# Optimization experiments

Hardware: AMD Instinct MI355X
Metric: run time of the kernel (lower is better)

## Reference

```python
import jax, jax.numpy as jnp
import numpy as np

B, N, D, H, FN, NL = 8, 512, 128, 64, 3, 3
OUT = 10


def setup_inputs() -> dict:
    key = jax.random.key(0)
    ks = jax.random.split(key, 20)
    X = jax.random.normal(ks[0], (B, N, D), dtype=jnp.float32)
    a = jax.random.uniform(ks[1], (B, N, N))
    A = (a < 0.02).astype(jnp.float32)
    A = jnp.maximum(A, jnp.swapaxes(A, 1, 2)) * (1.0 - jnp.eye(N, dtype=jnp.float32))
    w = lambda k, s: jax.random.normal(k, s, dtype=jnp.float32) * 0.05
    z = lambda s: jnp.zeros(s, jnp.float32)
    return {
        'X': X, 'A': A, 'p': 10,
        'curv_W1': w(ks[2], (D, H)), 'curv_b1': z((H,)),
        'curv_W2': w(ks[3], (H, 1)), 'curv_b2': z((1,)),
        'wm_W1': w(ks[4], (1, 64)), 'wm_b1': z((64,)),
        'wm_W2': w(ks[5], (64, 32)), 'wm_b2': z((32,)),
        'wm_W3': w(ks[6], (32, 1)), 'wm_b3': z((1,)),
        'fn_W1': w(ks[7], (FN, D, H)), 'fn_b1': z((FN, H)),
        'fn_W2': w(ks[8], (FN, H, 1)), 'fn_b2': z((FN, 1)),
        'gin_eps': z((NL,)),
        'gin0_W1': w(ks[9], (D, H)), 'gin0_b1': z((H,)),
        'gin0_W2': w(ks[10], (H, H)), 'gin0_b2': z((H,)),
        'gin1_W1': w(ks[11], (H, H)), 'gin1_b1': z((H,)),
        'gin1_W2': w(ks[12], (H, H)), 'gin1_b2': z((H,)),
        'gin2_W1': w(ks[13], (H, H)), 'gin2_b1': z((H,)),
        'gin2_W2': w(ks[14], (H, H)), 'gin2_b2': z((H,)),
        'out_W': w(ks[15], (D + H * NL, OUT)), 'out_b': z((OUT,)),
    }


def _curv_mlp(x, W1, b1, W2, b2):
    # MLP(nfeat->nhid->1) followed by sigmoid
    return jax.nn.sigmoid(jax.nn.relu(x @ W1 + b1) @ W2 + b2)


def _weight_mlp(A, W1, b1, W2, b2, W3, b3):
    # per-entry scalar MLP over adjacency: [B,N,N] -> [B,N,N]
    x = jax.nn.relu(A[..., None] * W1[0] + b1)  # [B,N,N,64]
    x = jax.nn.relu(x @ W2 + b2)                # [B,N,N,32]
    return jax.nn.sigmoid(x @ W3 + b3)[..., 0]


def _mv(w, v):
    return jnp.einsum('bij,bj->bi', w, v)


def _curvature_terms(f, w):
    # Algebraically identical to the torch O(N^2) expanded version, but
    # expressed with matvec contractions to avoid redundant [B,N,N] temps.
    deg = w.sum(axis=2)
    wf = _mv(w, f)
    # gamma_i = 0.5 sum_j w_ij (f_j - f_i)^2
    gamma = 0.5 * (f * f * deg - 2.0 * f * wf + _mv(w, f * f))
    # delta_f_i = sum_j w_ij (f_i - f_j)
    delta_f = f * deg - wf
    # delta_gamma_i = sum_j w_ij (gamma_i - gamma_j)
    delta_gamma = gamma * deg - _mv(w, gamma)
    # gfd_i = 0.5 sum_j w_ij (f_i - f_j)(delta_f_i - delta_f_j)
    gfd = 0.5 * (f * delta_f * deg - f * _mv(w, delta_f)
                 - delta_f * wf + _mv(w, f * delta_f))
    gamma2 = 0.5 * delta_gamma - gfd
    return gamma, gamma2


def _prune(A, kap, pct):
    num = int(N * pct / 100)  # static under jit (pct is a Python int)
    _, idx = jax.lax.top_k(kap, num)
    mask = jnp.ones((B, N), A.dtype).at[jnp.arange(B)[:, None], idx].set(0.0)
    return A * mask[:, :, None] * mask[:, None, :]


def _forward(X, A, curv_W1, curv_b1, curv_W2, curv_b2,
             wm_W1, wm_b1, wm_W2, wm_b2, wm_W3, wm_b3,
             fn_W1, fn_b1, fn_W2, fn_b2, gin_eps,
             gin0_W1, gin0_b1, gin0_W2, gin0_b2,
             gin1_W1, gin1_b1, gin1_W2, gin1_b2,
             gin2_W1, gin2_b1, gin2_W2, gin2_b2,
             out_W, out_b, p):
    kappa = _curv_mlp(X, curv_W1, curv_b1, curv_W2, curv_b2)  # [B,N,1]
    kap = kappa[..., 0]
    weights = _weight_mlp(A, wm_W1, wm_b1, wm_W2, wm_b2, wm_W3, wm_b3) * A
    curv_loss = jnp.float32(0.0)
    for i in range(FN):
        f = _curv_mlp(X, fn_W1[i], fn_b1[i], fn_W2[i], fn_b2[i])[..., 0]
        gamma, gamma2 = _curvature_terms(f, weights)
        curv_loss = curv_loss + jax.nn.relu(kap * gamma - gamma2).sum() - kappa.sum()
    gins = [(gin0_W1, gin0_b1, gin0_W2, gin0_b2),
            (gin1_W1, gin1_b1, gin1_W2, gin1_b2),
            (gin2_W1, gin2_b1, gin2_W2, gin2_b2)]
    h, A_cur, hiddens = X, A, [X]
    for t in range(NL):
        W1, b1, W2, b2 = gins[t]
        # GIN: MLP((1+eps) x + A x); dropout is identity (eval/deterministic)
        agg = (1.0 + gin_eps[t]) * h + jnp.einsum('bij,bjd->bid', A_cur, h)
        h = jax.nn.relu(jax.nn.relu(agg @ W1 + b1) @ W2 + b2)
        A_cur = _prune(A_cur, kap, p * (t + 1))
        hiddens.append(h)
    out = jnp.concatenate(hiddens, axis=2).sum(axis=1) @ out_W + out_b
    return out, curv_loss


def reference(X, A, p, curv_W1, curv_b1, curv_W2, curv_b2,
              wm_W1, wm_b1, wm_W2, wm_b2, wm_W3, wm_b3,
              fn_W1, fn_b1, fn_W2, fn_b2, gin_eps,
              gin0_W1, gin0_b1, gin0_W2, gin0_b2,
              gin1_W1, gin1_b1, gin1_W2, gin1_b2,
              gin2_W1, gin2_b1, gin2_W2, gin2_b2,
              out_W, out_b):
    return _forward(X, A, curv_W1, curv_b1, curv_W2, curv_b2,
                    wm_W1, wm_b1, wm_W2, wm_b2, wm_W3, wm_b3,
                    fn_W1, fn_b1, fn_W2, fn_b2, gin_eps,
                    gin0_W1, gin0_b1, gin0_W2, gin0_b2,
                    gin1_W1, gin1_b1, gin1_W2, gin1_b2,
                    gin2_W1, gin2_b1, gin2_W2, gin2_b2,
                    out_W, out_b, p)
```

## Files before the change

kernel.cpp:

```cpp
#include <hip/hip_runtime.h>
#include <math.h>

#define BATCH 8
#define NNODE 512
#define BN 4096
#define DIM 128
#define HID 64
#define CAP 64

__device__ __forceinline__ float sigmoidf(float x) {
  return 1.f / (1.f + expf(-x));
}
__device__ __forceinline__ float wave_sum(float v) {
  for (int off = 1; off < 64; off <<= 1) v += __shfl_xor(v, off, 64);
  return v;
}

template <int CIN, bool MASKED, int SOFF>
__device__ __forceinline__ void gin_block(
    float* smem, int node0, const float* hin, const float* W1g,
    const float* b1, const float* W2g, const float* b2, float eps1,
    const int* csr, const int* cnt, const float* mask, float* hout,
    float* Ssum) {
  float* W1s = smem;
  float* aggs = smem + CIN * HID;
  float* zs = aggs + 8 * CIN;
  int tid = threadIdx.x, wave = tid >> 6, lane = tid & 63;
  for (int t = tid; t < CIN * HID / 4; t += 256)
    ((float4*)W1s)[t] = ((const float4*)W1g)[t];
  for (int i = 0; i < 2; i++) {
    int ln = wave * 2 + i;
    int r = node0 + ln;
    int b9 = r & ~(NNODE - 1);
    const float* hi = hin + (size_t)r * CIN;
    float a0 = eps1 * hi[lane];
    float a1 = (CIN == 128) ? eps1 * hi[lane + 64] : 0.f;
    int n = cnt[r];
    const int* nb = csr + r * CAP;
    float mrow = MASKED ? mask[r] : 1.f;
    float s0 = 0.f, s1 = 0.f;
    for (int t = 0; t < n; t += 8) {
      int4 ja = *(const int4*)&nb[t];
      int4 jb = *(const int4*)&nb[t + 4];
      int r0 = b9 + ja.x, r1 = b9 + ja.y, r2 = b9 + ja.z, r3 = b9 + ja.w;
      int r4 = b9 + jb.x, r5 = b9 + jb.y, r6 = b9 + jb.z, r7 = b9 + jb.w;
      float m0 = MASKED ? mask[r0] : 1.f;
      float m1 = (t + 1 < n) ? (MASKED ? mask[r1] : 1.f) : 0.f;
      float m2 = (t + 2 < n) ? (MASKED ? mask[r2] : 1.f) : 0.f;
      float m3 = (t + 3 < n) ? (MASKED ? mask[r3] : 1.f) : 0.f;
      float m4 = (t + 4 < n) ? (MASKED ? mask[r4] : 1.f) : 0.f;
      float m5 = (t + 5 < n) ? (MASKED ? mask[r5] : 1.f) : 0.f;
      float m6 = (t + 6 < n) ? (MASKED ? mask[r6] : 1.f) : 0.f;
      float m7 = (t + 7 < n) ? (MASKED ? mask[r7] : 1.f) : 0.f;
      const float* p0 = hin + (size_t)r0 * CIN;
      const float* p1 = hin + (size_t)r1 * CIN;
      const float* p2 = hin + (size_t)r2 * CIN;
      const float* p3 = hin + (size_t)r3 * CIN;
      const float* p4 = hin + (size_t)r4 * CIN;
      const float* p5 = hin + (size_t)r5 * CIN;
      const float* p6 = hin + (size_t)r6 * CIN;
      const float* p7 = hin + (size_t)r7 * CIN;
      s0 += m0 * p0[lane] + m1 * p1[lane] + m2 * p2[lane] + m3 * p3[lane] +
            m4 * p4[lane] + m5 * p5[lane] + m6 * p6[lane] + m7 * p7[lane];
      if (CIN == 128)
        s1 += m0 * p0[lane + 64] + m1 * p1[lane + 64] + m2 * p2[lane + 64] +
              m3 * p3[lane + 64] + m4 * p4[lane + 64] + m5 * p5[lane + 64] +
              m6 * p6[lane + 64] + m7 * p7[lane + 64];
    }
    a0 += mrow * s0;
    if (CIN == 128) a1 += mrow * s1;
    aggs[ln * CIN + lane] = a0;
    if (CIN == 128) aggs[ln * CIN + 64 + lane] = a1;
  }
  __syncthreads();
  const float* x0 = aggs + (wave * 2 + 0) * CIN;
  const float* x1 = aggs + (wave * 2 + 1) * CIN;
  float bb = b1[lane];
  float acc0 = bb, acc1 = bb;
  for (int k = 0; k < CIN; k += 4) {
    float w0 = W1s[(k + 0) * HID + lane];
    float w1 = W1s[(k + 1) * HID + lane];
    float w2 = W1s[(k + 2) * HID + lane];
    float w3 = W1s[(k + 3) * HID + lane];
    float4 a;
    a = *(const float4*)&x0[k];
    acc0 += a.x * w0 + a.y * w1 + a.z * w2 + a.w * w3;
    a = *(const float4*)&x1[k];
    acc1 += a.x * w0 + a.y * w1 + a.z * w2 + a.w * w3;
  }
  zs[(wave * 2 + 0) * HID + lane] = fmaxf(0.f, acc0);
  zs[(wave * 2 + 1) * HID + lane] = fmaxf(0.f, acc1);
  const float* z0 = zs + (wave * 2 + 0) * HID;
  const float* z1 = zs + (wave * 2 + 1) * HID;
  float b2b = b2[lane];
  float c0 = b2b, c1v = b2b;
  for (int k = 0; k < HID; k += 4) {
    float w0 = W2g[(k + 0) * HID + lane];
    float w1 = W2g[(k + 1) * HID + lane];
    float w2 = W2g[(k + 2) * HID + lane];
    float w3 = W2g[(k + 3) * HID + lane];
    float4 a;
    a = *(const float4*)&z0[k];
    c0 += a.x * w0 + a.y * w1 + a.z * w2 + a.w * w3;
    a = *(const float4*)&z1[k];
    c1v += a.x * w0 + a.y * w1 + a.z * w2 + a.w * w3;
  }
  float h0 = fmaxf(0.f, c0), h1v = fmaxf(0.f, c1v);
  size_t rb = (size_t)(node0 + wave * 2) * HID + lane;
  hout[rb + 0 * HID] = h0;
  hout[rb + 1 * HID] = h1v;
  zs[(wave * 2) * HID + lane] = h0 + h1v;
  __syncthreads();
  if (tid < HID) {
    float tot = zs[0 * HID + tid] + zs[2 * HID + tid] + zs[4 * HID + tid] +
                zs[6 * HID + tid];
    atomicAdd(&Ssum[(node0 >> 9) * 320 + SOFF + tid], tot);
  }
}

__global__ __launch_bounds__(256) void k_stage1(
    const float* X, const float* A, const float* cW1, const float* cb1,
    const float* cW2, const float* cb2, const float* fW1, const float* fb1,
    const float* fW2, const float* fb2, const float* wm_W1, const float* wm_b1,
    const float* wm_W2, const float* wm_b2, const float* wm_W3,
    const float* wm_b3, float* kap, float* f, float* c1_out, int* csr,
    int* cnt_arr, float* deg, float* Ssum) {
  __shared__ float smem[10240];
  int bid = blockIdx.x;
  int tid = threadIdx.x, wave = tid >> 6, lane = tid & 63;
  if (bid < 1024) {
    int m = bid >> 8;
    int grp = bid & 255;
    float* W1s = smem;
    float* xs = smem + 8192;
    int node0 = grp * 16;
    const float* W1 = (m == 0) ? cW1 : fW1 + (size_t)(m - 1) * DIM * HID;
    for (int t = tid; t < 16 * DIM / 4; t += 256)
      ((float4*)xs)[t] = ((const float4*)(X + (size_t)node0 * DIM))[t];
    for (int t = tid; t < DIM * HID / 4; t += 256)
      ((float4*)W1s)[t] = ((const float4*)W1)[t];
    __syncthreads();
    const float* b1 = (m == 0) ? cb1 : fb1 + (m - 1) * HID;
    const float* W2 = (m == 0) ? cW2 : fW2 + (m - 1) * HID;
    float b2v = (m == 0) ? cb2[0] : fb2[m - 1];
    const float* x0 = xs + (wave * 4 + 0) * DIM;
    const float* x1 = xs + (wave * 4 + 1) * DIM;
    const float* x2 = xs + (wave * 4 + 2) * DIM;
    const float* x3 = xs + (wave * 4 + 3) * DIM;
    float w2l = W2[lane];
    float bb = b1[lane];
    float acc0 = bb, acc1 = bb, acc2 = bb, acc3 = bb;
    for (int k = 0; k < DIM; k += 4) {
      float w0 = W1s[(k + 0) * HID + lane];
      float w1 = W1s[(k + 1) * HID + lane];
      float w2 = W1s[(k + 2) * HID + lane];
      float w3 = W1s[(k + 3) * HID + lane];
      float4 a;
      a = *(const float4*)&x0[k];
      acc0 += a.x * w0 + a.y * w1 + a.z * w2 + a.w * w3;
      a = *(const float4*)&x1[k];
      acc1 += a.x * w0 + a.y * w1 + a.z * w2 + a.w * w3;
      a = *(const float4*)&x2[k];
      acc2 += a.x * w0 + a.y * w1 + a.z * w2 + a.w * w3;
      a = *(const float4*)&x3[k];
      acc3 += a.x * w0 + a.y * w1 + a.z * w2 + a.w * w3;
    }
    float s0 = wave_sum(fmaxf(0.f, acc0) * w2l);
    float s1 = wave_sum(fmaxf(0.f, acc1) * w2l);
    float s2 = wave_sum(fmaxf(0.f, acc2) * w2l);
    float s3 = wave_sum(fmaxf(0.f, acc3) * w2l);
    if (lane < 4) {
      float sv = (lane == 0) ? s0 : (lane == 1) ? s1 : (lane == 2) ? s2 : s3;
      float s = sigmoidf(sv + b2v);
      int node = node0 + wave * 4 + lane;
      if (m == 0) kap[node] = s;
      else f[node * 3 + (m - 1)] = s;
    }
    return;
  }
  if (bid < 2048) {
    int r = (bid - 1024) * 4 + wave;
    const float* row = A + (size_t)r * NNODE;
    int base = r * CAP, cnt = 0;
    for (int c = 0; c < NNODE / 64; c++) {
      int j = c * 64 + lane;
      bool nz = (row[j] != 0.f);
      unsigned long long mb = __ballot(nz);
      if (nz) {
        int pos = __popcll(mb & ((1ull << lane) - 1ull));
        int slot = cnt + pos;
        if (slot < CAP) csr[base + slot] = j;
      }
      cnt += (int)__popcll(mb);
    }
    int cc = cnt < CAP ? cnt : CAP;
    if (lane >= cc) csr[base + lane] = 0;
    if (lane == 0) {
      cnt_arr[r] = cc;
      deg[r] = (float)cnt;
    }
    return;
  }
  for (int t = tid; t < BATCH * 320; t += 256) Ssum[t] = 0.f;
  float* u = smem;
  float* y = smem + 64;
  int l = tid;
  if (l < 64) u[l] = fmaxf(0.f, wm_W1[l] + wm_b1[l]);
  __syncthreads();
  if (l < 32) {
    float a = wm_b2[l];
    for (int k = 0; k < 64; k++) a += u[k] * wm_W2[k * 32 + l];
    y[l] = fmaxf(0.f, a);
  }
  __syncthreads();
  if (l == 0) {
    float a = wm_b3[0];
    for (int k = 0; k < 32; k++) a += y[k] * wm_W3[k];
    *c1_out = sigmoidf(a);
  }
}

__global__ __launch_bounds__(256) void k_stage2(
    const float* X, const float* f, const float* kap, const int* p_ptr,
    const int* csr, const int* cnt, const float* deg, const float* c1p,
    const float* g0_W1, const float* g0_b1, const float* g0_W2,
    const float* g0_b2, const float* gin_eps, float* GG, float* M1, float* M2,
    float* h1, float* Ssum) {
  __shared__ float smem[9728];
  int bid = blockIdx.x;
  int wave = threadIdx.x >> 6, lane = threadIdx.x & 63;
  if (bid < 1024) {
    int r = bid * 4 + wave;
    int b9 = r & ~(NNODE - 1);
    int n = cnt[r];
    int j = csr[r * CAP + lane];
    float f0 = 0.f, f1 = 0.f, f2 = 0.f;
    if (lane < n) {
      const float* fj = f + (size_t)(b9 + j) * 3;
      f0 = fj[0]; f1 = fj[1]; f2 = fj[2];
    }
    float s10 = wave_sum(f0), s11 = wave_sum(f1), s12 = wave_sum(f2);
    float s20 = wave_sum(f0 * f0), s21 = wave_sum(f1 * f1),
          s22 = wave_sum(f2 * f2);
    if (lane < 3) {
      float s1 = (lane == 0) ? s10 : (lane == 1) ? s11 : s12;
      float s2 = (lane == 0) ? s20 : (lane == 1) ? s21 : s22;
      float c1 = *c1p, dA = deg[r];
      float fi = f[r * 3 + lane];
      float gamma = 0.5f * c1 * (fi * fi * dA - 2.f * fi * s1 + s2);
      float df = c1 * (fi * dA - s1);
      float* o = GG + (size_t)r * 12;
      o[lane * 3 + 0] = gamma;
      o[lane * 3 + 1] = df;
      o[lane * 3 + 2] = fi * df;
      o[9 + lane] = s1;
    }
    return;
  }
  if (bid < 1024 + BATCH) {
    int b = bid - 1024;
    float* ks = smem;
    for (int t = threadIdx.x; t < NNODE; t += 256) ks[t] = kap[b * NNODE + t];
    __syncthreads();
    int p = *p_ptr;
    int num1 = (NNODE * p) / 100;
    int num2 = (NNODE * 2 * p) / 100;
    int numm = num1 > num2 ? num1 : num2;
    for (int i = threadIdx.x; i < NNODE; i += 256) {
      float v = ks[i];
      int rank = 0;
      for (int j = 0; j < NNODE; j++) {
        float u = ks[j];
        rank += (u > v) || (u == v && j < i);
      }
      M1[b * NNODE + i] = (rank < num1) ? 0.f : 1.f;
      M2[b * NNODE + i] = (rank < numm) ? 0.f : 1.f;
    }
    return;
  }
  if (bid < 1024 + BATCH + 512) {
    gin_block<DIM, false, 128>(smem, (bid - 1024 - BATCH) * 8, X, g0_W1,
                               g0_b1, g0_W2, g0_b2, 1.f + gin_eps[0], csr,
                               cnt, nullptr, h1, Ssum);
    return;
  }
  int idx = bid - (1024 + BATCH + 512);
  int b = idx >> 3, sl = idx & 7;
  int col = threadIdx.x & 127, rg = threadIdx.x >> 7;
  const float* xb = X + (size_t)b * NNODE * DIM;
  int n0 = sl * 64;
  float s = 0.f;
  for (int n = n0 + rg; n < n0 + 64; n += 2) s += xb[(size_t)n * DIM + col];
  smem[threadIdx.x] = s;
  __syncthreads();
  if (threadIdx.x < 128)
    atomicAdd(&Ssum[b * 320 + col], smem[threadIdx.x] + smem[threadIdx.x + 128]);
}

__global__ __launch_bounds__(256) void k_stage3(
    const float* f, const float* kap, const float* deg, const float* GG,
    const int* csr, const int* cnt, const float* c1p, float* loss_part,
    const float* h1, const float* g1_W1, const float* g1_b1,
    const float* g1_W2, const float* g1_b2, const float* gin_eps,
    const float* M1, float* h2, float* Ssum) {
  __shared__ float smem[5120];
  __shared__ float part[4];
  int bid = blockIdx.x;
  int wave = threadIdx.x >> 6, lane = threadIdx.x & 63;
  if (bid < 1024) {
    int r = bid * 4 + wave;
    int b9 = r & ~(NNODE - 1);
    int n = cnt[r];
    int j = csr[r * CAP + lane];
    float T[9];
    for (int c = 0; c < 9; c++) T[c] = 0.f;
    if (lane < n) {
      const float4* g = (const float4*)(GG + (size_t)(b9 + j) * 12);
      float4 g0 = g[0], g1 = g[1], g2 = g[2];
      T[0] = g0.x; T[1] = g0.y; T[2] = g0.z;
      T[3] = g0.w; T[4] = g1.x; T[5] = g1.y;
      T[6] = g1.z; T[7] = g1.w; T[8] = g2.x;
    }
    for (int c = 0; c < 9; c++) T[c] = wave_sum(T[c]);
    float kp = kap[r];
    float local = 0.f;
    if (lane < 3) {
      int i = lane;
      float c1 = *c1p, dA = deg[r];
      const float* o = GG + (size_t)r * 12;
      float fi = f[r * 3 + i];
      float s1 = o[9 + i];
      float gamma = o[i * 3 + 0], df = o[i * 3 + 1];
      float dgamma = c1 * (gamma * dA - T[i * 3 + 0]);
      float gfd = 0.5f * c1 * (fi * df * dA - fi * T[i * 3 + 1] - df * s1 +
                               T[i * 3 + 2]);
      float gamma2 = 0.5f * dgamma - gfd;
      local = fmaxf(0.f, kp * gamma - gamma2);
    }
    if (lane == 0) local -= 3.f * kp;
    local = wave_sum(local);
    if (lane == 0) part[wave] = local;
    __syncthreads();
    if (threadIdx.x == 0)
      loss_part[bid] = part[0] + part[1] + part[2] + part[3];
    return;
  }
  gin_block<HID, true, 192>(smem, (bid - 1024) * 8, h1, g1_W1, g1_b1, g1_W2,
                            g1_b2, 1.f + gin_eps[1], csr, cnt, M1, h2, Ssum);
}

__global__ __launch_bounds__(256) void k_stage4(
    const float* h2, const float* g2_W1, const float* g2_b1,
    const float* g2_W2, const float* g2_b2, const float* gin_eps,
    const int* csr, const int* cnt, const float* M2, float* h3, float* Ssum) {
  __shared__ float smem[5120];
  gin_block<HID, true, 256>(smem, blockIdx.x * 8, h2, g2_W1, g2_b1, g2_W2,
                            g2_b2, 1.f + gin_eps[2], csr, cnt, M2, h3, Ssum);
}

__global__ __launch_bounds__(320) void k_out(
    const float* Ssum, const float* out_W, const float* out_b,
    const float* loss_part, float* out) {
  int b = blockIdx.x;
  int t = threadIdx.x;
  __shared__ float S[320];
  __shared__ float wpart[5];
  S[t] = Ssum[b * 320 + t];
  if (b == 0) {
    float ls = 0.f;
    for (int i = t; i < 1024; i += 320) ls += loss_part[i];
    ls = wave_sum(ls);
    if ((t & 63) == 0) wpart[t >> 6] = ls;
  }
  __syncthreads();
  if (t < 10) {
    float acc = out_b[t];
    for (int d = 0; d < 320; d++) acc += S[d] * out_W[d * 10 + t];
    out[b * 10 + t] = acc;
  }
  if (b == 0 && t == 0) {
    float ls = 0.f;
    for (int w = 0; w < 5; w++) ls += wpart[w];
    out[80] = ls;
  }
}

extern "C" void kernel_launch(void* const* d_in, const int* in_sizes, int n_in,
                              void* d_out, int out_size, void* d_ws,
                              size_t ws_size, hipStream_t stream) {
  const float* X       = (const float*)d_in[0];
  const float* A       = (const float*)d_in[1];
  const int*   p       = (const int*)d_in[2];
  const float* curv_W1 = (const float*)d_in[3];
  const float* curv_b1 = (const float*)d_in[4];
  const float* curv_W2 = (const float*)d_in[5];
  const float* curv_b2 = (const float*)d_in[6];
  const float* wm_W1   = (const float*)d_in[7];
  const float* wm_b1   = (const float*)d_in[8];
  const float* wm_W2   = (const float*)d_in[9];
  const float* wm_b2   = (const float*)d_in[10];
  const float* wm_W3   = (const float*)d_in[11];
  const float* wm_b3   = (const float*)d_in[12];
  const float* fn_W1   = (const float*)d_in[13];
  const float* fn_b1   = (const float*)d_in[14];
  const float* fn_W2   = (const float*)d_in[15];
  const float* fn_b2   = (const float*)d_in[16];
  const float* gin_eps = (const float*)d_in[17];
  const float* g0_W1   = (const float*)d_in[18];
  const float* g0_b1   = (const float*)d_in[19];
  const float* g0_W2   = (const float*)d_in[20];
  const float* g0_b2   = (const float*)d_in[21];
  const float* g1_W1   = (const float*)d_in[22];
  const float* g1_b1   = (const float*)d_in[23];
  const float* g1_W2   = (const float*)d_in[24];
  const float* g1_b2   = (const float*)d_in[25];
  const float* g2_W1   = (const float*)d_in[26];
  const float* g2_b1   = (const float*)d_in[27];
  const float* g2_W2   = (const float*)d_in[28];
  const float* g2_b2   = (const float*)d_in[29];
  const float* out_W   = (const float*)d_in[30];
  const float* out_b   = (const float*)d_in[31];
  float* out = (float*)d_out;

  float* ws = (float*)d_ws;
  size_t o = 0;
  float* loss_part = ws + o; o += 1024;
  float* c1       = ws + o; o += 16;
  float* Ssum     = ws + o; o += BATCH * 320 + 16;
  float* kap      = ws + o; o += BN;
  float* f        = ws + o; o += (size_t)BN * 3 + 16;
  float* deg      = ws + o; o += BN;
  float* M1       = ws + o; o += BN;
  float* M2       = ws + o; o += BN;
  float* GG       = ws + o; o += (size_t)BN * 12;
  float* h1       = ws + o; o += (size_t)BN * HID;
  float* h2       = ws + o; o += (size_t)BN * HID;
  float* h3       = ws + o; o += (size_t)BN * HID;
  int* cnt  = (int*)(ws + o); o += BN;
  int* csr  = (int*)(ws + o); o += (size_t)BN * CAP;

  k_stage1<<<2049, 256, 0, stream>>>(
      X, A, curv_W1, curv_b1, curv_W2, curv_b2, fn_W1, fn_b1, fn_W2, fn_b2,
      wm_W1, wm_b1, wm_W2, wm_b2, wm_W3, wm_b3, kap, f, c1, csr, cnt, deg,
      Ssum);
  k_stage2<<<1024 + BATCH + 512 + 64, 256, 0, stream>>>(
      X, f, kap, p, csr, cnt, deg, c1, g0_W1, g0_b1, g0_W2, g0_b2, gin_eps,
      GG, M1, M2, h1, Ssum);
  k_stage3<<<1536, 256, 0, stream>>>(f, kap, deg, GG, csr, cnt, c1, loss_part,
                                     h1, g1_W1, g1_b1, g1_W2, g1_b2, gin_eps,
                                     M1, h2, Ssum);
  k_stage4<<<512, 256, 0, stream>>>(h2, g2_W1, g2_b1, g2_W2, g2_b2, gin_eps,
                                    csr, cnt, M2, h3, Ssum);
  k_out<<<BATCH, 320, 0, stream>>>(Ssum, out_W, out_b, loss_part, out);
}
```

Measured before the change: 200.5 us.

## Replace shared-memory weight staging with wave shuffles and direct global weight reads

Removes the per-block copies of W1 and of X/aggregate rows into LDS in the stage-1 MLP and in gin_block. Activations now stay in registers and are broadcast with __shfl, while weights are read straight from global/L2 each iteration. Neighbour gathers now load the CSR indices once per wave and broadcast them by shuffle, processing two rows together. LDS use drops to at most 512 floats per block, which should allow more resident blocks. In exchange there are many more cross-lane shuffles and repeated global weight loads with no reuse through shared memory.

```diff
diff --git a/kernel.cpp b/kernel.cpp
--- a/kernel.cpp
+++ b/kernel.cpp
@@ -18,102 +18,79 @@
 
 template <int CIN, bool MASKED, int SOFF>
 __device__ __forceinline__ void gin_block(
-    float* smem, int node0, const float* hin, const float* W1g,
+    float* zsum, int node0, const float* hin, const float* W1g,
     const float* b1, const float* W2g, const float* b2, float eps1,
     const int* csr, const int* cnt, const float* mask, float* hout,
     float* Ssum) {
-  float* W1s = smem;
-  float* aggs = smem + CIN * HID;
-  float* zs = aggs + 8 * CIN;
   int tid = threadIdx.x, wave = tid >> 6, lane = tid & 63;
-  for (int t = tid; t < CIN * HID / 4; t += 256)
-    ((float4*)W1s)[t] = ((const float4*)W1g)[t];
-  for (int i = 0; i < 2; i++) {
-    int ln = wave * 2 + i;
-    int r = node0 + ln;
-    int b9 = r & ~(NNODE - 1);
-    const float* hi = hin + (size_t)r * CIN;
-    float a0 = eps1 * hi[lane];
-    float a1 = (CIN == 128) ? eps1 * hi[lane + 64] : 0.f;
-    int n = cnt[r];
-    const int* nb = csr + r * CAP;
-    float mrow = MASKED ? mask[r] : 1.f;
-    float s0 = 0.f, s1 = 0.f;
-    for (int t = 0; t < n; t += 8) {
-      int4 ja = *(const int4*)&nb[t];
-      int4 jb = *(const int4*)&nb[t + 4];
-      int r0 = b9 + ja.x, r1 = b9 + ja.y, r2 = b9 + ja.z, r3 = b9 + ja.w;
-      int r4 = b9 + jb.x, r5 = b9 + jb.y, r6 = b9 + jb.z, r7 = b9 + jb.w;
-      float m0 = MASKED ? mask[r0] : 1.f;
-      float m1 = (t + 1 < n) ? (MASKED ? mask[r1] : 1.f) : 0.f;
-      float m2 = (t + 2 < n) ? (MASKED ? mask[r2] : 1.f) : 0.f;
-      float m3 = (t + 3 < n) ? (MASKED ? mask[r3] : 1.f) : 0.f;
-      float m4 = (t + 4 < n) ? (MASKED ? mask[r4] : 1.f) : 0.f;
-      float m5 = (t + 5 < n) ? (MASKED ? mask[r5] : 1.f) : 0.f;
-      float m6 = (t + 6 < n) ? (MASKED ? mask[r6] : 1.f) : 0.f;
-      float m7 = (t + 7 < n) ? (MASKED ? mask[r7] : 1.f) : 0.f;
-      const float* p0 = hin + (size_t)r0 * CIN;
-      const float* p1 = hin + (size_t)r1 * CIN;
-      const float* p2 = hin + (size_t)r2 * CIN;
-      const float* p3 = hin + (size_t)r3 * CIN;
-      const float* p4 = hin + (size_t)r4 * CIN;
-      const float* p5 = hin + (size_t)r5 * CIN;
-      const float* p6 = hin + (size_t)r6 * CIN;
-      const float* p7 = hin + (size_t)r7 * CIN;
-      s0 += m0 * p0[lane] + m1 * p1[lane] + m2 * p2[lane] + m3 * p3[lane] +
-            m4 * p4[lane] + m5 * p5[lane] + m6 * p6[lane] + m7 * p7[lane];
-      if (CIN == 128)
-        s1 += m0 * p0[lane + 64] + m1 * p1[lane + 64] + m2 * p2[lane + 64] +
-              m3 * p3[lane + 64] + m4 * p4[lane + 64] + m5 * p5[lane + 64] +
-              m6 * p6[lane + 64] + m7 * p7[lane + 64];
-    }
-    a0 += mrow * s0;
-    if (CIN == 128) a1 += mrow * s1;
-    aggs[ln * CIN + lane] = a0;
-    if (CIN == 128) aggs[ln * CIN + 64 + lane] = a1;
-  }
+  int r0 = node0 + wave * 2, r1 = r0 + 1;
+  int b9 = r0 & ~(NNODE - 1);
+  int n0 = cnt[r0], n1 = cnt[r1];
+  int jv0 = csr[r0 * CAP + lane];
+  int jv1 = csr[r1 * CAP + lane];
+  float mv0, mv1;
+  if (MASKED) {
+    mv0 = (lane < n0) ? mask[b9 + jv0] : 0.f;
+    mv1 = (lane < n1) ? mask[b9 + jv1] : 0.f;
+  } else {
+    mv0 = (lane < n0) ? 1.f : 0.f;
+    mv1 = (lane < n1) ? 1.f : 0.f;
+  }
+  float mrow0 = MASKED ? mask[r0] : 1.f;
+  float mrow1 = MASKED ? mask[r1] : 1.f;
+  const float* h0p = hin + (size_t)r0 * CIN;
+  const float* h1p = hin + (size_t)r1 * CIN;
+  float a00 = eps1 * h0p[lane];
+  float a01 = (CIN == 128) ? eps1 * h0p[lane + 64] : 0.f;
+  float a10 = eps1 * h1p[lane];
+  float a11 = (CIN == 128) ? eps1 * h1p[lane + 64] : 0.f;
+  float s00 = 0.f, s01 = 0.f, s10 = 0.f, s11 = 0.f;
+  int nm = n0 > n1 ? n0 : n1;
+  for (int t = 0; t < nm; t++) {
+    int j0 = __shfl(jv0, t, 64);
+    int j1 = __shfl(jv1, t, 64);
+    float m0 = __shfl(mv0, t, 64);
+    float m1 = __shfl(mv1, t, 64);
+    const float* p0 = hin + (size_t)(b9 + j0) * CIN;
+    const float* p1 = hin + (size_t)(b9 + j1) * CIN;
+    s00 += m0 * p0[lane];
+    s10 += m1 * p1[lane];
+    if (CIN == 128) {
+      s01 += m0 * p0[lane + 64];
+      s11 += m1 * p1[lane + 64];
+    }
+  }
+  a00 += mrow0 * s00;
+  a10 += mrow1 * s10;
+  if (CIN == 128) { a01 += mrow0 * s01; a11 += mrow1 * s11; }
+  float z0 = b1[lane], z1 = z0;
+  for (int k = 0; k < 64; k++) {
+    float w = W1g[k * HID + lane];
+    z0 += __shfl(a00, k, 64) * w;
+    z1 += __shfl(a10, k, 64) * w;
+  }
+  if (CIN == 128) {
+    for (int k = 0; k < 64; k++) {
+      float w = W1g[(k + 64) * HID + lane];
+      z0 += __shfl(a01, k, 64) * w;
+      z1 += __shfl(a11, k, 64) * w;
+    }
+  }
+  z0 = fmaxf(0.f, z0);
+  z1 = fmaxf(0.f, z1);
+  float c0 = b2[lane], c1v = c0;
+  for (int k = 0; k < 64; k++) {
+    float w = W2g[k * HID + lane];
+    c0 += __shfl(z0, k, 64) * w;
+    c1v += __shfl(z1, k, 64) * w;
+  }
+  float o0 = fmaxf(0.f, c0), o1 = fmaxf(0.f, c1v);
+  hout[(size_t)r0 * HID + lane] = o0;
+  hout[(size_t)r1 * HID + lane] = o1;
+  zsum[wave * 64 + lane] = o0 + o1;
   __syncthreads();
-  const float* x0 = aggs + (wave * 2 + 0) * CIN;
-  const float* x1 = aggs + (wave * 2 + 1) * CIN;
-  float bb = b1[lane];
-  float acc0 = bb, acc1 = bb;
-  for (int k = 0; k < CIN; k += 4) {
-    float w0 = W1s[(k + 0) * HID + lane];
-    float w1 = W1s[(k + 1) * HID + lane];
-    float w2 = W1s[(k + 2) * HID + lane];
-    float w3 = W1s[(k + 3) * HID + lane];
-    float4 a;
-    a = *(const float4*)&x0[k];
-    acc0 += a.x * w0 + a.y * w1 + a.z * w2 + a.w * w3;
-    a = *(const float4*)&x1[k];
-    acc1 += a.x * w0 + a.y * w1 + a.z * w2 + a.w * w3;
-  }
-  zs[(wave * 2 + 0) * HID + lane] = fmaxf(0.f, acc0);
-  zs[(wave * 2 + 1) * HID + lane] = fmaxf(0.f, acc1);
-  const float* z0 = zs + (wave * 2 + 0) * HID;
-  const float* z1 = zs + (wave * 2 + 1) * HID;
-  float b2b = b2[lane];
-  float c0 = b2b, c1v = b2b;
-  for (int k = 0; k < HID; k += 4) {
-    float w0 = W2g[(k + 0) * HID + lane];
-    float w1 = W2g[(k + 1) * HID + lane];
-    float w2 = W2g[(k + 2) * HID + lane];
-    float w3 = W2g[(k + 3) * HID + lane];
-    float4 a;
-    a = *(const float4*)&z0[k];
-    c0 += a.x * w0 + a.y * w1 + a.z * w2 + a.w * w3;
-    a = *(const float4*)&z1[k];
-    c1v += a.x * w0 + a.y * w1 + a.z * w2 + a.w * w3;
-  }
-  float h0 = fmaxf(0.f, c0), h1v = fmaxf(0.f, c1v);
-  size_t rb = (size_t)(node0 + wave * 2) * HID + lane;
-  hout[rb + 0 * HID] = h0;
-  hout[rb + 1 * HID] = h1v;
-  zs[(wave * 2) * HID + lane] = h0 + h1v;
-  __syncthreads();
-  if (tid < HID) {
-    float tot = zs[0 * HID + tid] + zs[2 * HID + tid] + zs[4 * HID + tid] +
-                zs[6 * HID + tid];
+  if (tid < 64) {
+    float tot = zsum[tid] + zsum[64 + tid] + zsum[128 + tid] + zsum[192 + tid];
     atomicAdd(&Ssum[(node0 >> 9) * 320 + SOFF + tid], tot);
   }
 }
@@ -125,46 +102,39 @@
     const float* wm_W2, const float* wm_b2, const float* wm_W3,
     const float* wm_b3, float* kap, float* f, float* c1_out, int* csr,
     int* cnt_arr, float* deg, float* Ssum) {
-  __shared__ float smem[10240];
+  __shared__ float sbuf[512];
   int bid = blockIdx.x;
   int tid = threadIdx.x, wave = tid >> 6, lane = tid & 63;
   if (bid < 1024) {
     int m = bid >> 8;
     int grp = bid & 255;
-    float* W1s = smem;
-    float* xs = smem + 8192;
-    int node0 = grp * 16;
+    int nb = grp * 16 + wave * 4;
     const float* W1 = (m == 0) ? cW1 : fW1 + (size_t)(m - 1) * DIM * HID;
-    for (int t = tid; t < 16 * DIM / 4; t += 256)
-      ((float4*)xs)[t] = ((const float4*)(X + (size_t)node0 * DIM))[t];
-    for (int t = tid; t < DIM * HID / 4; t += 256)
-      ((float4*)W1s)[t] = ((const float4*)W1)[t];
-    __syncthreads();
     const float* b1 = (m == 0) ? cb1 : fb1 + (m - 1) * HID;
     const float* W2 = (m == 0) ? cW2 : fW2 + (m - 1) * HID;
     float b2v = (m == 0) ? cb2[0] : fb2[m - 1];
-    const float* x0 = xs + (wave * 4 + 0) * DIM;
-    const float* x1 = xs + (wave * 4 + 1) * DIM;
-    const float* x2 = xs + (wave * 4 + 2) * DIM;
-    const float* x3 = xs + (wave * 4 + 3) * DIM;
-    float w2l = W2[lane];
+    const float* xp = X + (size_t)nb * DIM;
+    float x0a = xp[lane],       x0b = xp[64 + lane];
+    float x1a = xp[128 + lane], x1b = xp[192 + lane];
+    float x2a = xp[256 + lane], x2b = xp[320 + lane];
+    float x3a = xp[384 + lane], x3b = xp[448 + lane];
     float bb = b1[lane];
     float acc0 = bb, acc1 = bb, acc2 = bb, acc3 = bb;
-    for (int k = 0; k < DIM; k += 4) {
-      float w0 = W1s[(k + 0) * HID + lane];
-      float w1 = W1s[(k + 1) * HID + lane];
-      float w2 = W1s[(k + 2) * HID + lane];
-      float w3 = W1s[(k + 3) * HID + lane];
-      float4 a;
-      a = *(const float4*)&x0[k];
-      acc0 += a.x * w0 + a.y * w1 + a.z * w2 + a.w * w3;
-      a = *(const float4*)&x1[k];
-      acc1 += a.x * w0 + a.y * w1 + a.z * w2 + a.w * w3;
-      a = *(const float4*)&x2[k];
-      acc2 += a.x * w0 + a.y * w1 + a.z * w2 + a.w * w3;
-      a = *(const float4*)&x3[k];
-      acc3 += a.x * w0 + a.y * w1 + a.z * w2 + a.w * w3;
-    }
+    for (int k = 0; k < 64; k++) {
+      float w = W1[k * HID + lane];
+      acc0 += __shfl(x0a, k, 64) * w;
+      acc1 += __shfl(x1a, k, 64) * w;
+      acc2 += __shfl(x2a, k, 64) * w;
+      acc3 += __shfl(x3a, k, 64) * w;
+    }
+    for (int k = 0; k < 64; k++) {
+      float w = W1[(k + 64) * HID + lane];
+      acc0 += __shfl(x0b, k, 64) * w;
+      acc1 += __shfl(x1b, k, 64) * w;
+      acc2 += __shfl(x2b, k, 64) * w;
+      acc3 += __shfl(x3b, k, 64) * w;
+    }
+    float w2l = W2[lane];
     float s0 = wave_sum(fmaxf(0.f, acc0) * w2l);
     float s1 = wave_sum(fmaxf(0.f, acc1) * w2l);
     float s2 = wave_sum(fmaxf(0.f, acc2) * w2l);
@@ -172,7 +142,7 @@
     if (lane < 4) {
       float sv = (lane == 0) ? s0 : (lane == 1) ? s1 : (lane == 2) ? s2 : s3;
       float s = sigmoidf(sv + b2v);
-      int node = node0 + wave * 4 + lane;
+      int node = nb + lane;
       if (m == 0) kap[node] = s;
       else f[node * 3 + (m - 1)] = s;
     }
@@ -202,8 +172,8 @@
     return;
   }
   for (int t = tid; t < BATCH * 320; t += 256) Ssum[t] = 0.f;
-  float* u = smem;
-  float* y = smem + 64;
+  float* u = sbuf;
+  float* y = sbuf + 64;
   int l = tid;
   if (l < 64) u[l] = fmaxf(0.f, wm_W1[l] + wm_b1[l]);
   __syncthreads();
@@ -226,7 +196,7 @@
     const float* g0_W1, const float* g0_b1, const float* g0_W2,
     const float* g0_b2, const float* gin_eps, float* GG, float* M1, float* M2,
     float* h1, float* Ssum) {
-  __shared__ float smem[9728];
+  __shared__ float sbuf[512];
   int bid = blockIdx.x;
   int wave = threadIdx.x >> 6, lane = threadIdx.x & 63;
   if (bid < 1024) {
@@ -259,7 +229,7 @@
   }
   if (bid < 1024 + BATCH) {
     int b = bid - 1024;
-    float* ks = smem;
+    float* ks = sbuf;
     for (int t = threadIdx.x; t < NNODE; t += 256) ks[t] = kap[b * NNODE + t];
     __syncthreads();
     int p = *p_ptr;
@@ -279,7 +249,7 @@
     return;
   }
   if (bid < 1024 + BATCH + 512) {
-    gin_block<DIM, false, 128>(smem, (bid - 1024 - BATCH) * 8, X, g0_W1,
+    gin_block<DIM, false, 128>(sbuf, (bid - 1024 - BATCH) * 8, X, g0_W1,
                                g0_b1, g0_W2, g0_b2, 1.f + gin_eps[0], csr,
                                cnt, nullptr, h1, Ssum);
     return;
@@ -291,10 +261,10 @@
   int n0 = sl * 64;
   float s = 0.f;
   for (int n = n0 + rg; n < n0 + 64; n += 2) s += xb[(size_t)n * DIM + col];
-  smem[threadIdx.x] = s;
+  sbuf[threadIdx.x] = s;
   __syncthreads();
   if (threadIdx.x < 128)
-    atomicAdd(&Ssum[b * 320 + col], smem[threadIdx.x] + smem[threadIdx.x + 128]);
+    atomicAdd(&Ssum[b * 320 + col], sbuf[threadIdx.x] + sbuf[threadIdx.x + 128]);
 }
 
 __global__ __launch_bounds__(256) void k_stage3(
@@ -303,8 +273,7 @@
     const float* h1, const float* g1_W1, const float* g1_b1,
     const float* g1_W2, const float* g1_b2, const float* gin_eps,
     const float* M1, float* h2, float* Ssum) {
-  __shared__ float smem[5120];
-  __shared__ float part[4];
+  __shared__ float sbuf[260];
   int bid = blockIdx.x;
   int wave = threadIdx.x >> 6, lane = threadIdx.x & 63;
   if (bid < 1024) {
@@ -339,13 +308,13 @@
     }
     if (lane == 0) local -= 3.f * kp;
     local = wave_sum(local);
-    if (lane == 0) part[wave] = local;
+    if (lane == 0) sbuf[256 + wave] = local;
     __syncthreads();
     if (threadIdx.x == 0)
-      loss_part[bid] = part[0] + part[1] + part[2] + part[3];
-    return;
-  }
-  gin_block<HID, true, 192>(smem, (bid - 1024) * 8, h1, g1_W1, g1_b1, g1_W2,
+      loss_part[bid] = sbuf[256] + sbuf[257] + sbuf[258] + sbuf[259];
+    return;
+  }
+  gin_block<HID, true, 192>(sbuf, (bid - 1024) * 8, h1, g1_W1, g1_b1, g1_W2,
                             g1_b2, 1.f + gin_eps[1], csr, cnt, M1, h2, Ssum);
 }
 
@@ -353,8 +322,8 @@
     const float* h2, const float* g2_W1, const float* g2_b1,
     const float* g2_W2, const float* g2_b2, const float* gin_eps,
     const int* csr, const int* cnt, const float* M2, float* h3, float* Ssum) {
-  __shared__ float smem[5120];
-  gin_block<HID, true, 256>(smem, blockIdx.x * 8, h2, g2_W1, g2_b1, g2_W2,
+  __shared__ float sbuf[256];
+  gin_block<HID, true, 256>(sbuf, blockIdx.x * 8, h2, g2_W1, g2_b1, g2_W2,
                             g2_b2, 1.f + gin_eps[2], csr, cnt, M2, h3, Ssum);
 }
 
```

Result: slower. 219.5 us (+9.5%).

## Fuse output head into last GIN kernel and move input column sums to stage one

Applied to the files above, without the earlier changes.

Removes the separate k_out launch. Instead, the last block of k_stage4 to finish, detected with a global done counter and atomicAdd, computes the final linear head and sums the loss. The per-batch column sum of X moves from 64 atomic-accumulating blocks in stage 2 to 8 blocks in stage 1 that write directly without atomics. This saves a kernel launch and some atomics. It adds a serial tail in one block, and there is a possible ordering race between the block that zeroes Ssum and the blocks that write the X sums.

```diff
diff --git a/kernel.cpp b/kernel.cpp
--- a/kernel.cpp
+++ b/kernel.cpp
@@ -124,7 +124,7 @@
     const float* fW2, const float* fb2, const float* wm_W1, const float* wm_b1,
     const float* wm_W2, const float* wm_b2, const float* wm_W3,
     const float* wm_b3, float* kap, float* f, float* c1_out, int* csr,
-    int* cnt_arr, float* deg, float* Ssum) {
+    int* cnt_arr, float* deg, float* Ssum, int* done) {
   __shared__ float smem[10240];
   int bid = blockIdx.x;
   int tid = threadIdx.x, wave = tid >> 6, lane = tid & 63;
@@ -201,22 +201,38 @@
     }
     return;
   }
-  for (int t = tid; t < BATCH * 320; t += 256) Ssum[t] = 0.f;
-  float* u = smem;
-  float* y = smem + 64;
-  int l = tid;
-  if (l < 64) u[l] = fmaxf(0.f, wm_W1[l] + wm_b1[l]);
-  __syncthreads();
-  if (l < 32) {
-    float a = wm_b2[l];
-    for (int k = 0; k < 64; k++) a += u[k] * wm_W2[k * 32 + l];
-    y[l] = fmaxf(0.f, a);
-  }
-  __syncthreads();
-  if (l == 0) {
-    float a = wm_b3[0];
-    for (int k = 0; k < 32; k++) a += y[k] * wm_W3[k];
-    *c1_out = sigmoidf(a);
+  if (bid == 2048) {
+    for (int t = tid; t < BATCH * 320; t += 256) Ssum[t] = 0.f;
+    if (tid == 0) *done = 0;
+    float* u = smem;
+    float* y = smem + 64;
+    int l = tid;
+    if (l < 64) u[l] = fmaxf(0.f, wm_W1[l] + wm_b1[l]);
+    __syncthreads();
+    if (l < 32) {
+      float a = wm_b2[l];
+      for (int k = 0; k < 64; k++) a += u[k] * wm_W2[k * 32 + l];
+      y[l] = fmaxf(0.f, a);
+    }
+    __syncthreads();
+    if (l == 0) {
+      float a = wm_b3[0];
+      for (int k = 0; k < 32; k++) a += y[k] * wm_W3[k];
+      *c1_out = sigmoidf(a);
+    }
+    return;
+  }
+  int idx = bid - 2049;
+  if (idx >= BATCH) return;
+  int b = idx;
+  int col = threadIdx.x & 127, rg = threadIdx.x >> 7;
+  const float* xb = X + (size_t)b * NNODE * DIM;
+  float s = 0.f;
+  for (int n = rg; n < NNODE; n += 2) s += xb[(size_t)n * DIM + col];
+  smem[threadIdx.x] = s;
+  __syncthreads();
+  if (threadIdx.x < 128) {
+    Ssum[b * 320 + col] = smem[threadIdx.x] + smem[threadIdx.x + 128];
   }
 }
 
@@ -278,23 +294,9 @@
     }
     return;
   }
-  if (bid < 1024 + BATCH + 512) {
-    gin_block<DIM, false, 128>(smem, (bid - 1024 - BATCH) * 8, X, g0_W1,
-                               g0_b1, g0_W2, g0_b2, 1.f + gin_eps[0], csr,
-                               cnt, nullptr, h1, Ssum);
-    return;
-  }
-  int idx = bid - (1024 + BATCH + 512);
-  int b = idx >> 3, sl = idx & 7;
-  int col = threadIdx.x & 127, rg = threadIdx.x >> 7;
-  const float* xb = X + (size_t)b * NNODE * DIM;
-  int n0 = sl * 64;
-  float s = 0.f;
-  for (int n = n0 + rg; n < n0 + 64; n += 2) s += xb[(size_t)n * DIM + col];
-  smem[threadIdx.x] = s;
-  __syncthreads();
-  if (threadIdx.x < 128)
-    atomicAdd(&Ssum[b * 320 + col], smem[threadIdx.x] + smem[threadIdx.x + 128]);
+  gin_block<DIM, false, 128>(smem, (bid - 1024 - BATCH) * 8, X, g0_W1, g0_b1,
+                             g0_W2, g0_b2, 1.f + gin_eps[0], csr, cnt,
+                             nullptr, h1, Ssum);
 }
 
 __global__ __launch_bounds__(256) void k_stage3(
@@ -352,37 +354,38 @@
 __global__ __launch_bounds__(256) void k_stage4(
     const float* h2, const float* g2_W1, const float* g2_b1,
     const float* g2_W2, const float* g2_b2, const float* gin_eps,
-    const int* csr, const int* cnt, const float* M2, float* h3, float* Ssum) {
+    const int* csr, const int* cnt, const float* M2, float* h3, float* Ssum,
+    int* done, const float* loss_part, const float* out_W, const float* out_b,
+    float* out) {
   __shared__ float smem[5120];
+  __shared__ int is_last;
   gin_block<HID, true, 256>(smem, blockIdx.x * 8, h2, g2_W1, g2_b1, g2_W2,
                             g2_b2, 1.f + gin_eps[2], csr, cnt, M2, h3, Ssum);
-}
-
-__global__ __launch_bounds__(320) void k_out(
-    const float* Ssum, const float* out_W, const float* out_b,
-    const float* loss_part, float* out) {
-  int b = blockIdx.x;
+  __syncthreads();
+  if (threadIdx.x == 0) {
+    __threadfence();
+    is_last = (atomicAdd(done, 1) == gridDim.x - 1);
+  }
+  __syncthreads();
+  if (!is_last) return;
   int t = threadIdx.x;
-  __shared__ float S[320];
-  __shared__ float wpart[5];
-  S[t] = Ssum[b * 320 + t];
-  if (b == 0) {
-    float ls = 0.f;
-    for (int i = t; i < 1024; i += 320) ls += loss_part[i];
-    ls = wave_sum(ls);
-    if ((t & 63) == 0) wpart[t >> 6] = ls;
-  }
-  __syncthreads();
-  if (t < 10) {
-    float acc = out_b[t];
-    for (int d = 0; d < 320; d++) acc += S[d] * out_W[d * 10 + t];
-    out[b * 10 + t] = acc;
-  }
-  if (b == 0 && t == 0) {
-    float ls = 0.f;
-    for (int w = 0; w < 5; w++) ls += wpart[w];
-    out[80] = ls;
-  }
+  float* S = smem;
+  for (int i = t; i < BATCH * 320; i += 256)
+    S[i] = atomicAdd(&Ssum[i], 0.f);
+  float ls = 0.f;
+  for (int i = t; i < 1024; i += 256) ls += loss_part[i];
+  ls = wave_sum(ls);
+  if ((t & 63) == 0) smem[2560 + (t >> 6)] = ls;
+  __syncthreads();
+  if (t < 80) {
+    int b = t / 10, oc = t % 10;
+    float acc = out_b[oc];
+    const float* Sb = S + b * 320;
+    for (int d = 0; d < 320; d++) acc += Sb[d] * out_W[d * 10 + oc];
+    out[b * 10 + oc] = acc;
+  }
+  if (t == 0)
+    out[80] = smem[2560] + smem[2561] + smem[2562] + smem[2563];
 }
 
 extern "C" void kernel_launch(void* const* d_in, const int* in_sizes, int n_in,
@@ -437,19 +440,20 @@
   float* h2       = ws + o; o += (size_t)BN * HID;
   float* h3       = ws + o; o += (size_t)BN * HID;
   int* cnt  = (int*)(ws + o); o += BN;
+  int* done = (int*)(ws + o); o += 16;
   int* csr  = (int*)(ws + o); o += (size_t)BN * CAP;
 
-  k_stage1<<<2049, 256, 0, stream>>>(
+  k_stage1<<<2049 + BATCH, 256, 0, stream>>>(
       X, A, curv_W1, curv_b1, curv_W2, curv_b2, fn_W1, fn_b1, fn_W2, fn_b2,
       wm_W1, wm_b1, wm_W2, wm_b2, wm_W3, wm_b3, kap, f, c1, csr, cnt, deg,
-      Ssum);
-  k_stage2<<<1024 + BATCH + 512 + 64, 256, 0, stream>>>(
+      Ssum, done);
+  k_stage2<<<1024 + BATCH + 512, 256, 0, stream>>>(
       X, f, kap, p, csr, cnt, deg, c1, g0_W1, g0_b1, g0_W2, g0_b2, gin_eps,
       GG, M1, M2, h1, Ssum);
   k_stage3<<<1536, 256, 0, stream>>>(f, kap, deg, GG, csr, cnt, c1, loss_part,
                                      h1, g1_W1, g1_b1, g1_W2, g1_b2, gin_eps,
                                      M1, h2, Ssum);
   k_stage4<<<512, 256, 0, stream>>>(h2, g2_W1, g2_b1, g2_W2, g2_b2, gin_eps,
-                                    csr, cnt, M2, h3, Ssum);
-  k_out<<<BATCH, 320, 0, stream>>>(Ssum, out_W, out_b, loss_part, out);
-}
+                                    csr, cnt, M2, h3, Ssum, done, loss_part,
+                                    out_W, out_b, out);
+}
```

Result: slower. 268.4 us (+33.9%).

## Fuse curvature loss into one block per graph using shared memory

Applied to the files above, without the earlier changes.

The two-pass curvature computation (gamma/delta terms, then neighbor sums of them) was split across stage2 and stage3 with 1024 wave-per-node blocks each and a global GG buffer. Both passes now run inside stage2 in 8 blocks, one per graph, with f and the per-node terms kept in shared memory and a block sync between passes. This drops the GG global round-trip and the loss work in stage3, and shrinks the loss reduction to 8 partials. The cost is that only 8 blocks do this serial per-thread neighbor loop, which may become the tail of stage2.

```diff
diff --git a/kernel.cpp b/kernel.cpp
--- a/kernel.cpp
+++ b/kernel.cpp
@@ -224,49 +224,106 @@
     const float* X, const float* f, const float* kap, const int* p_ptr,
     const int* csr, const int* cnt, const float* deg, const float* c1p,
     const float* g0_W1, const float* g0_b1, const float* g0_W2,
-    const float* g0_b2, const float* gin_eps, float* GG, float* M1, float* M2,
-    float* h1, float* Ssum) {
+    const float* g0_b2, const float* gin_eps, float* loss_part, float* M1,
+    float* M2, float* h1, float* Ssum) {
   __shared__ float smem[9728];
   int bid = blockIdx.x;
-  int wave = threadIdx.x >> 6, lane = threadIdx.x & 63;
-  if (bid < 1024) {
-    int r = bid * 4 + wave;
-    int b9 = r & ~(NNODE - 1);
-    int n = cnt[r];
-    int j = csr[r * CAP + lane];
-    float f0 = 0.f, f1 = 0.f, f2 = 0.f;
-    if (lane < n) {
-      const float* fj = f + (size_t)(b9 + j) * 3;
-      f0 = fj[0]; f1 = fj[1]; f2 = fj[2];
-    }
-    float s10 = wave_sum(f0), s11 = wave_sum(f1), s12 = wave_sum(f2);
-    float s20 = wave_sum(f0 * f0), s21 = wave_sum(f1 * f1),
-          s22 = wave_sum(f2 * f2);
-    if (lane < 3) {
-      float s1 = (lane == 0) ? s10 : (lane == 1) ? s11 : s12;
-      float s2 = (lane == 0) ? s20 : (lane == 1) ? s21 : s22;
-      float c1 = *c1p, dA = deg[r];
-      float fi = f[r * 3 + lane];
-      float gamma = 0.5f * c1 * (fi * fi * dA - 2.f * fi * s1 + s2);
-      float df = c1 * (fi * dA - s1);
-      float* o = GG + (size_t)r * 12;
-      o[lane * 3 + 0] = gamma;
-      o[lane * 3 + 1] = df;
-      o[lane * 3 + 2] = fi * df;
-      o[9 + lane] = s1;
-    }
+  int tid = threadIdx.x;
+  int wave = tid >> 6, lane = tid & 63;
+  if (bid < BATCH) {
+    int b = bid;
+    float* fv = smem;
+    float* ggv = smem + 1536;
+    float* s1v = smem + 6144;
+    float* part = smem + 7680;
+    for (int t = tid; t < NNODE * 3; t += 256)
+      fv[t] = f[b * NNODE * 3 + t];
+    __syncthreads();
+    float c1 = *c1p;
+    for (int rr = 0; rr < 2; rr++) {
+      int r = tid * 2 + rr;
+      int gr = b * NNODE + r;
+      int n = cnt[gr];
+      const int* nb = csr + gr * CAP;
+      float s1[3] = {0, 0, 0}, s2[3] = {0, 0, 0};
+      for (int t = 0; t < n; t += 4) {
+        int4 j4 = *(const int4*)&nb[t];
+        float w1 = (t + 1 < n) ? 1.f : 0.f;
+        float w2 = (t + 2 < n) ? 1.f : 0.f;
+        float w3 = (t + 3 < n) ? 1.f : 0.f;
+        const float* p0 = &fv[j4.x * 3];
+        const float* p1 = &fv[j4.y * 3];
+        const float* p2 = &fv[j4.z * 3];
+        const float* p3 = &fv[j4.w * 3];
+        for (int i = 0; i < 3; i++) {
+          float v0 = p0[i], v1 = p1[i], v2 = p2[i], v3 = p3[i];
+          s1[i] += v0 + w1 * v1 + w2 * v2 + w3 * v3;
+          s2[i] += v0 * v0 + w1 * v1 * v1 + w2 * v2 * v2 + w3 * v3 * v3;
+        }
+      }
+      float dA = deg[gr];
+      for (int i = 0; i < 3; i++) {
+        float fi = fv[r * 3 + i];
+        float gamma = 0.5f * c1 * (fi * fi * dA - 2.f * fi * s1[i] + s2[i]);
+        float df = c1 * (fi * dA - s1[i]);
+        ggv[r * 9 + i * 3 + 0] = gamma;
+        ggv[r * 9 + i * 3 + 1] = df;
+        ggv[r * 9 + i * 3 + 2] = fi * df;
+        s1v[r * 3 + i] = s1[i];
+      }
+    }
+    __syncthreads();
+    float local = 0.f;
+    for (int rr = 0; rr < 2; rr++) {
+      int r = tid * 2 + rr;
+      int gr = b * NNODE + r;
+      int n = cnt[gr];
+      const int* nb = csr + gr * CAP;
+      float T[9];
+      for (int c = 0; c < 9; c++) T[c] = 0.f;
+      for (int t = 0; t < n; t += 4) {
+        int4 j4 = *(const int4*)&nb[t];
+        float w1 = (t + 1 < n) ? 1.f : 0.f;
+        float w2 = (t + 2 < n) ? 1.f : 0.f;
+        float w3 = (t + 3 < n) ? 1.f : 0.f;
+        const float* g0 = &ggv[j4.x * 9];
+        const float* g1 = &ggv[j4.y * 9];
+        const float* g2 = &ggv[j4.z * 9];
+        const float* g3 = &ggv[j4.w * 9];
+        for (int c = 0; c < 9; c++)
+          T[c] += g0[c] + w1 * g1[c] + w2 * g2[c] + w3 * g3[c];
+      }
+      float dA = deg[gr];
+      float kp = kap[gr];
+      for (int i = 0; i < 3; i++) {
+        float fi = fv[r * 3 + i];
+        float s1 = s1v[r * 3 + i];
+        float gamma = ggv[r * 9 + i * 3 + 0];
+        float df = ggv[r * 9 + i * 3 + 1];
+        float dgamma = c1 * (gamma * dA - T[i * 3 + 0]);
+        float gfd = 0.5f * c1 * (fi * df * dA - fi * T[i * 3 + 1] -
+                                 df * s1 + T[i * 3 + 2]);
+        float gamma2 = 0.5f * dgamma - gfd;
+        local += fmaxf(0.f, kp * gamma - gamma2);
+      }
+      local -= 3.f * kp;
+    }
+    local = wave_sum(local);
+    if (lane == 0) part[wave] = local;
+    __syncthreads();
+    if (tid == 0) loss_part[b] = part[0] + part[1] + part[2] + part[3];
     return;
   }
-  if (bid < 1024 + BATCH) {
-    int b = bid - 1024;
+  if (bid < 2 * BATCH) {
+    int b = bid - BATCH;
     float* ks = smem;
-    for (int t = threadIdx.x; t < NNODE; t += 256) ks[t] = kap[b * NNODE + t];
+    for (int t = tid; t < NNODE; t += 256) ks[t] = kap[b * NNODE + t];
     __syncthreads();
     int p = *p_ptr;
     int num1 = (NNODE * p) / 100;
     int num2 = (NNODE * 2 * p) / 100;
     int numm = num1 > num2 ? num1 : num2;
-    for (int i = threadIdx.x; i < NNODE; i += 256) {
+    for (int i = tid; i < NNODE; i += 256) {
       float v = ks[i];
       int rank = 0;
       for (int j = 0; j < NNODE; j++) {
@@ -278,74 +335,31 @@
     }
     return;
   }
-  if (bid < 1024 + BATCH + 512) {
-    gin_block<DIM, false, 128>(smem, (bid - 1024 - BATCH) * 8, X, g0_W1,
-                               g0_b1, g0_W2, g0_b2, 1.f + gin_eps[0], csr,
-                               cnt, nullptr, h1, Ssum);
+  if (bid < 2 * BATCH + 512) {
+    gin_block<DIM, false, 128>(smem, (bid - 2 * BATCH) * 8, X, g0_W1, g0_b1,
+                               g0_W2, g0_b2, 1.f + gin_eps[0], csr, cnt,
+                               nullptr, h1, Ssum);
     return;
   }
-  int idx = bid - (1024 + BATCH + 512);
+  int idx = bid - (2 * BATCH + 512);
   int b = idx >> 3, sl = idx & 7;
-  int col = threadIdx.x & 127, rg = threadIdx.x >> 7;
+  int col = tid & 127, rg = tid >> 7;
   const float* xb = X + (size_t)b * NNODE * DIM;
   int n0 = sl * 64;
   float s = 0.f;
   for (int n = n0 + rg; n < n0 + 64; n += 2) s += xb[(size_t)n * DIM + col];
-  smem[threadIdx.x] = s;
-  __syncthreads();
-  if (threadIdx.x < 128)
-    atomicAdd(&Ssum[b * 320 + col], smem[threadIdx.x] + smem[threadIdx.x + 128]);
+  smem[tid] = s;
+  __syncthreads();
+  if (tid < 128)
+    atomicAdd(&Ssum[b * 320 + col], smem[tid] + smem[tid + 128]);
 }
 
 __global__ __launch_bounds__(256) void k_stage3(
-    const float* f, const float* kap, const float* deg, const float* GG,
-    const int* csr, const int* cnt, const float* c1p, float* loss_part,
     const float* h1, const float* g1_W1, const float* g1_b1,
     const float* g1_W2, const float* g1_b2, const float* gin_eps,
-    const float* M1, float* h2, float* Ssum) {
+    const int* csr, const int* cnt, const float* M1, float* h2, float* Ssum) {
   __shared__ float smem[5120];
-  __shared__ float part[4];
-  int bid = blockIdx.x;
-  int wave = threadIdx.x >> 6, lane = threadIdx.x & 63;
-  if (bid < 1024) {
-    int r = bid * 4 + wave;
-    int b9 = r & ~(NNODE - 1);
-    int n = cnt[r];
-    int j = csr[r * CAP + lane];
-    float T[9];
-    for (int c = 0; c < 9; c++) T[c] = 0.f;
-    if (lane < n) {
-      const float4* g = (const float4*)(GG + (size_t)(b9 + j) * 12);
-      float4 g0 = g[0], g1 = g[1], g2 = g[2];
-      T[0] = g0.x; T[1] = g0.y; T[2] = g0.z;
-      T[3] = g0.w; T[4] = g1.x; T[5] = g1.y;
-      T[6] = g1.z; T[7] = g1.w; T[8] = g2.x;
-    }
-    for (int c = 0; c < 9; c++) T[c] = wave_sum(T[c]);
-    float kp = kap[r];
-    float local = 0.f;
-    if (lane < 3) {
-      int i = lane;
-      float c1 = *c1p, dA = deg[r];
-      const float* o = GG + (size_t)r * 12;
-      float fi = f[r * 3 + i];
-      float s1 = o[9 + i];
-      float gamma = o[i * 3 + 0], df = o[i * 3 + 1];
-      float dgamma = c1 * (gamma * dA - T[i * 3 + 0]);
-      float gfd = 0.5f * c1 * (fi * df * dA - fi * T[i * 3 + 1] - df * s1 +
-                               T[i * 3 + 2]);
-      float gamma2 = 0.5f * dgamma - gfd;
-      local = fmaxf(0.f, kp * gamma - gamma2);
-    }
-    if (lane == 0) local -= 3.f * kp;
-    local = wave_sum(local);
-    if (lane == 0) part[wave] = local;
-    __syncthreads();
-    if (threadIdx.x == 0)
-      loss_part[bid] = part[0] + part[1] + part[2] + part[3];
-    return;
-  }
-  gin_block<HID, true, 192>(smem, (bid - 1024) * 8, h1, g1_W1, g1_b1, g1_W2,
+  gin_block<HID, true, 192>(smem, blockIdx.x * 8, h1, g1_W1, g1_b1, g1_W2,
                             g1_b2, 1.f + gin_eps[1], csr, cnt, M1, h2, Ssum);
 }
 
@@ -364,14 +378,7 @@
   int b = blockIdx.x;
   int t = threadIdx.x;
   __shared__ float S[320];
-  __shared__ float wpart[5];
   S[t] = Ssum[b * 320 + t];
-  if (b == 0) {
-    float ls = 0.f;
-    for (int i = t; i < 1024; i += 320) ls += loss_part[i];
-    ls = wave_sum(ls);
-    if ((t & 63) == 0) wpart[t >> 6] = ls;
-  }
   __syncthreads();
   if (t < 10) {
     float acc = out_b[t];
@@ -380,7 +387,7 @@
   }
   if (b == 0 && t == 0) {
     float ls = 0.f;
-    for (int w = 0; w < 5; w++) ls += wpart[w];
+    for (int i = 0; i < BATCH; i++) ls += loss_part[i];
     out[80] = ls;
   }
 }
@@ -424,7 +431,7 @@
 
   float* ws = (float*)d_ws;
   size_t o = 0;
-  float* loss_part = ws + o; o += 1024;
+  float* loss_part = ws + o; o += 16;
   float* c1       = ws + o; o += 16;
   float* Ssum     = ws + o; o += BATCH * 320 + 16;
   float* kap      = ws + o; o += BN;
@@ -432,7 +439,6 @@
   float* deg      = ws + o; o += BN;
   float* M1       = ws + o; o += BN;
   float* M2       = ws + o; o += BN;
-  float* GG       = ws + o; o += (size_t)BN * 12;
   float* h1       = ws + o; o += (size_t)BN * HID;
   float* h2       = ws + o; o += (size_t)BN * HID;
   float* h3       = ws + o; o += (size_t)BN * HID;
@@ -443,12 +449,11 @@
       X, A, curv_W1, curv_b1, curv_W2, curv_b2, fn_W1, fn_b1, fn_W2, fn_b2,
       wm_W1, wm_b1, wm_W2, wm_b2, wm_W3, wm_b3, kap, f, c1, csr, cnt, deg,
       Ssum);
-  k_stage2<<<1024 + BATCH + 512 + 64, 256, 0, stream>>>(
+  k_stage2<<<2 * BATCH + 512 + 64, 256, 0, stream>>>(
       X, f, kap, p, csr, cnt, deg, c1, g0_W1, g0_b1, g0_W2, g0_b2, gin_eps,
-      GG, M1, M2, h1, Ssum);
-  k_stage3<<<1536, 256, 0, stream>>>(f, kap, deg, GG, csr, cnt, c1, loss_part,
-                                     h1, g1_W1, g1_b1, g1_W2, g1_b2, gin_eps,
-                                     M1, h2, Ssum);
+      loss_part, M1, M2, h1, Ssum);
+  k_stage3<<<512, 256, 0, stream>>>(h1, g1_W1, g1_b1, g1_W2, g1_b2, gin_eps,
+                                    csr, cnt, M1, h2, Ssum);
   k_stage4<<<512, 256, 0, stream>>>(h2, g2_W1, g2_b1, g2_W2, g2_b2, gin_eps,
                                     csr, cnt, M2, h3, Ssum);
   k_out<<<BATCH, 320, 0, stream>>>(Ssum, out_W, out_b, loss_part, out);
```

Measured after the change: 199.4 us. No clear change (-0.5%).
